# Kernel tuning notes

Hardware: AMD Instinct MI355X
Metric: run time of the kernel (lower is better)

## Reference

```python
import jax, jax.numpy as jnp
import numpy as np

D_MODEL = 512
H = 8
DK = D_MODEL // H  # 64


def setup_inputs() -> dict:
    key = jax.random.key(0)
    ks = jax.random.split(key, 8)
    B, S = 2, 4096
    q = jax.random.normal(ks[0], (B, S, D_MODEL), dtype=jnp.float32)
    k = jax.random.normal(ks[1], (B, S, D_MODEL), dtype=jnp.float32)
    v = jax.random.normal(ks[2], (B, S, D_MODEL), dtype=jnp.float32)
    # per-head projection weights, torch nn.Linear layout [out, in], stacked over heads
    scale = 1.0 / np.sqrt(D_MODEL)
    Wq = jax.random.uniform(ks[3], (H, DK, D_MODEL), jnp.float32, -scale, scale)
    Wk = jax.random.uniform(ks[4], (H, DK, D_MODEL), jnp.float32, -scale, scale)
    Wv = jax.random.uniform(ks[5], (H, DK, D_MODEL), jnp.float32, -scale, scale)
    Wo = jax.random.uniform(ks[6], (D_MODEL, D_MODEL), jnp.float32, -scale, scale)
    # causal mask (True = keep), matches masked_fill(mask.logical_not(), -inf)
    mask = jnp.tril(jnp.ones((S, S), dtype=jnp.bool_))
    return {"q": q, "k": k, "v": v, "Wq": Wq, "Wk": Wk, "Wv": Wv, "Wo": Wo, "mask": mask}


def reference(q, k, v, Wq, Wk, Wv, Wo, mask):
    # per-head projections (stacked): x @ W^T for each head -> [B, H, S, DK]
    qh = jnp.einsum('bsd,hed->bhse', q, Wq)
    kh = jnp.einsum('bsd,hed->bhse', k, Wk)
    vh = jnp.einsum('bsd,hed->bhse', v, Wv)
    scaling = 1.0 / np.sqrt(DK)
    scores = jnp.einsum('bhse,bhte->bhst', qh, kh) * scaling  # [B,H,S,S]
    scores = jnp.where(mask, scores, -jnp.inf)
    attn = jax.nn.softmax(scores, axis=-1)
    heads = jnp.einsum('bhst,bhte->bhse', attn, vh)  # [B,H,S,DK]
    B, _, S, _ = heads.shape
    concat = jnp.transpose(heads, (0, 2, 1, 3)).reshape(B, S, D_MODEL)
    return concat @ Wo.T
```

## Files before the change

### kernel.cpp

```cpp
#include <hip/hip_runtime.h>
#include <hip/hip_bf16.h>
#include <math.h>

typedef __bf16 bf16_t;
typedef __bf16 bf16x8 __attribute__((ext_vector_type(8)));
typedef __bf16 bf16x4 __attribute__((ext_vector_type(4)));
typedef short short4v __attribute__((ext_vector_type(4)));
typedef float f32x4 __attribute__((ext_vector_type(4)));

__device__ __forceinline__ f32x4 mfma_k32(bf16x8 a, bf16x8 b, f32x4 c) {
    return __builtin_amdgcn_mfma_f32_16x16x32_bf16(a, b, c, 0, 0, 0);
}

__device__ __forceinline__ f32x4 mfma_k16(bf16x4 a, bf16x4 b, f32x4 c) {
#if __has_builtin(__builtin_amdgcn_mfma_f32_16x16x16_bf16)
    return __builtin_amdgcn_mfma_f32_16x16x16_bf16(a, b, c, 0, 0, 0);
#elif __has_builtin(__builtin_amdgcn_mfma_f32_16x16x16bf16_1k)
    short4v as, bs;
    __builtin_memcpy(&as, &a, 8);
    __builtin_memcpy(&bs, &b, 8);
    return __builtin_amdgcn_mfma_f32_16x16x16bf16_1k(as, bs, c, 0, 0, 0);
#else
    f32x4 d = c;
    asm volatile("v_mfma_f32_16x16x16_bf16 %0, %1, %2, %0" : "+v"(d) : "v"(a), "v"(b));
    return d;
#endif
}

__device__ __forceinline__ void async16(const bf16_t* g, __bf16* l) {
    __builtin_amdgcn_global_load_lds(
        (const __attribute__((address_space(1))) void*)g,
        (__attribute__((address_space(3))) void*)l, 16, 0, 0);
}

__device__ __forceinline__ int swz_col(int col, int row) {
    return (col & ~63) | ((((col >> 3) & 7) ^ (row & 7)) << 3) | (col & 7);
}

__global__ __launch_bounds__(256) void cvt_x(const float* __restrict__ q,
                                             const float* __restrict__ k,
                                             const float* __restrict__ v,
                                             bf16_t* __restrict__ qc,
                                             bf16_t* __restrict__ kc,
                                             bf16_t* __restrict__ vc) {
    size_t i = ((size_t)blockIdx.x * 256 + threadIdx.x) * 8;
    int row = (int)(i >> 9), col = (int)(i & 511);
    size_t di = (size_t)row * 512 + swz_col(col, row);
    float4 a0 = *(const float4*)(q + i), a1 = *(const float4*)(q + i + 4);
    float4 b0 = *(const float4*)(k + i), b1 = *(const float4*)(k + i + 4);
    float4 c0 = *(const float4*)(v + i), c1 = *(const float4*)(v + i + 4);
    bf16x8 qo, ko, vo;
    qo[0]=(__bf16)a0.x; qo[1]=(__bf16)a0.y; qo[2]=(__bf16)a0.z; qo[3]=(__bf16)a0.w;
    qo[4]=(__bf16)a1.x; qo[5]=(__bf16)a1.y; qo[6]=(__bf16)a1.z; qo[7]=(__bf16)a1.w;
    ko[0]=(__bf16)b0.x; ko[1]=(__bf16)b0.y; ko[2]=(__bf16)b0.z; ko[3]=(__bf16)b0.w;
    ko[4]=(__bf16)b1.x; ko[5]=(__bf16)b1.y; ko[6]=(__bf16)b1.z; ko[7]=(__bf16)b1.w;
    vo[0]=(__bf16)c0.x; vo[1]=(__bf16)c0.y; vo[2]=(__bf16)c0.z; vo[3]=(__bf16)c0.w;
    vo[4]=(__bf16)c1.x; vo[5]=(__bf16)c1.y; vo[6]=(__bf16)c1.z; vo[7]=(__bf16)c1.w;
    *(bf16x8*)(qc + di) = qo;
    *(bf16x8*)(kc + di) = ko;
    *(bf16x8*)(vc + di) = vo;
}

__global__ __launch_bounds__(256) void cvt_w(const float* __restrict__ Wq,
                                             const float* __restrict__ Wk,
                                             const float* __restrict__ Wv,
                                             const float* __restrict__ Wo,
                                             bf16_t* __restrict__ Wc) {
    const int m = blockIdx.y;
    const float* src = m == 0 ? Wq : m == 1 ? Wk : m == 2 ? Wv : Wo;
    const float sc = (m == 0) ? 0.125f * 1.44269504088896f : 1.0f;
    size_t i = ((size_t)blockIdx.x * 256 + threadIdx.x) * 8;
    int row = (int)(i >> 9), col = (int)(i & 511);
    float4 a0 = *(const float4*)(src + i), a1 = *(const float4*)(src + i + 4);
    bf16x8 o;
    o[0]=(__bf16)(a0.x*sc); o[1]=(__bf16)(a0.y*sc); o[2]=(__bf16)(a0.z*sc); o[3]=(__bf16)(a0.w*sc);
    o[4]=(__bf16)(a1.x*sc); o[5]=(__bf16)(a1.y*sc); o[6]=(__bf16)(a1.z*sc); o[7]=(__bf16)(a1.w*sc);
    *(bf16x8*)(Wc + (size_t)m * 262144 + (size_t)row * 512 + swz_col(col, row)) = o;
}

template<int MODE>
__global__ __launch_bounds__(256) void gemm_nt(const bf16_t* __restrict__ A,
                                               const bf16_t* __restrict__ B,
                                               void* __restrict__ outp) {
    __shared__ __bf16 Asm[64 * 64];
    __shared__ __bf16 Bsm[64 * 64];
    const int tid  = threadIdx.x;
    const int wave = tid >> 6;
    const int lane = tid & 63;
    const int quad = lane >> 4;
    const int l16  = lane & 15;
    const int swz  = l16 & 7;
    const int m0 = blockIdx.x * 64;
    const int n0 = blockIdx.y * 64;
    const int r8 = lane >> 3;
    const int c8 = (lane & 7) * 8;

    f32x4 acc[4];
    for (int i = 0; i < 4; ++i) acc[i] = (f32x4){0.f, 0.f, 0.f, 0.f};

    for (int kt = 0; kt < 512; kt += 64) {
        __syncthreads();
        for (int j = 0; j < 2; ++j) {
            int row = wave * 16 + j * 8 + r8;
            async16(A + (size_t)(m0 + row) * 512 + kt + c8, &Asm[(wave * 16 + j * 8) * 64]);
            async16(B + (size_t)(n0 + row) * 512 + kt + c8, &Bsm[(wave * 16 + j * 8) * 64]);
        }
        __syncthreads();

        for (int ks = 0; ks < 2; ++ks) {
            bf16x8 afr = *(const bf16x8*)&Asm[(wave * 16 + l16) * 64 + ((ks * 4 + quad) ^ swz) * 8];
            for (int nt = 0; nt < 4; ++nt) {
                bf16x8 bfr = *(const bf16x8*)&Bsm[(nt * 16 + l16) * 64 + ((ks * 4 + quad) ^ swz) * 8];
                acc[nt] = mfma_k32(afr, bfr, acc[nt]);
            }
        }
    }

    if (MODE == 0) {
        bf16_t* out = (bf16_t*)outp;
        for (int nt = 0; nt < 4; ++nt) {
            int e = n0 + nt * 16 + l16;
            int h = e >> 6, el = e & 63;
            for (int r = 0; r < 4; ++r) {
                int row = m0 + wave * 16 + quad * 4 + r;
                int b = row >> 12, s = row & 4095;
                int elp = (((el >> 3) ^ (row & 7)) << 3) | (el & 7);
                out[(((size_t)(b * 8 + h)) * 4096 + s) * 64 + elp] = (bf16_t)acc[nt][r];
            }
        }
    } else if (MODE == 1) {
        bf16_t* out = (bf16_t*)outp;
        for (int nt = 0; nt < 4; ++nt) {
            int s_g = n0 + nt * 16 + l16;
            int b = s_g >> 12, sl = s_g & 4095;
            int f = 16 * (l16 >> 2) + 4 * nt + (l16 & 3);
            for (int r = 0; r < 4; ++r) {
                int e_g = m0 + wave * 16 + quad * 4 + r;
                int h = e_g >> 6, el = e_g & 63;
                int p = (sl & ~63) | ((((f >> 3) ^ (e_g & 7)) & 7) << 3) | (f & 7);
                out[(((size_t)(b * 8 + h)) * 64 + el) * 4096 + p] = (bf16_t)acc[nt][r];
            }
        }
    } else {
        float* out = (float*)outp;
        for (int nt = 0; nt < 4; ++nt) {
            int n = n0 + nt * 16 + l16;
            for (int r = 0; r < 4; ++r) {
                int row = m0 + wave * 16 + quad * 4 + r;
                out[(size_t)row * 512 + n] = acc[nt][r];
            }
        }
    }
}

__global__ __launch_bounds__(256) void attn_kernel(const bf16_t* __restrict__ qh,
                                                   const bf16_t* __restrict__ kh,
                                                   const bf16_t* __restrict__ vh,
                                                   bf16_t* __restrict__ ao) {
    __shared__ __bf16 Ksm[64 * 64];
    __shared__ __bf16 VTsm[64 * 64];
    const int tid  = threadIdx.x;
    const int wave = tid >> 6;
    const int lane = tid & 63;
    const int quad = lane >> 4;
    const int l16  = lane & 15;
    const int swz  = l16 & 7;
    const int bh   = blockIdx.y;
    const size_t base = (size_t)bh * 4096 * 64;
    const int r8 = lane >> 3;
    const int c8 = (lane & 7) * 8;
    const int b = bh >> 3, h = bh & 7;

    for (int leg = 0; leg < 2; ++leg) {
        const int qt = leg ? (63 - (int)blockIdx.x) : (int)blockIdx.x;
        const int q0 = qt * 64;
        const int qrow = wave * 16 + l16;
        const bf16_t* qp = qh + base + (size_t)(q0 + qrow) * 64;
        bf16x8 qf0 = *(const bf16x8*)(qp + ((quad ^ swz) * 8));
        bf16x8 qf1 = *(const bf16x8*)(qp + (((4 + quad) ^ swz) * 8));

        f32x4 o[4];
        for (int i = 0; i < 4; ++i) o[i] = (f32x4){0.f, 0.f, 0.f, 0.f};
        float lsum = 0.f;

        for (int jt = 0; jt <= qt; ++jt) {
            const int j0 = jt * 64;
            __syncthreads();
            for (int j = 0; j < 2; ++j) {
                int row = wave * 16 + j * 8 + r8;
                async16(kh + base + (size_t)(j0 + row) * 64 + c8,
                        &Ksm[(wave * 16 + j * 8) * 64]);
                async16(vh + (size_t)(bh * 64 + row) * 4096 + j0 + c8,
                        &VTsm[(wave * 16 + j * 8) * 64]);
            }
            __syncthreads();

            f32x4 st[4];
            for (int nt = 0; nt < 4; ++nt) {
                bf16x8 kf0 = *(const bf16x8*)&Ksm[(nt * 16 + l16) * 64 + ((quad ^ swz) * 8)];
                bf16x8 kf1 = *(const bf16x8*)&Ksm[(nt * 16 + l16) * 64 + (((4 + quad) ^ swz) * 8)];
                f32x4 z = (f32x4){0.f, 0.f, 0.f, 0.f};
                z = mfma_k32(kf0, qf0, z);
                z = mfma_k32(kf1, qf1, z);
                st[nt] = z;
            }

            bf16x4 pf[4];
            if (jt == qt) {
                for (int nt = 0; nt < 4; ++nt)
                    for (int r = 0; r < 4; ++r) {
                        int key = nt * 16 + quad * 4 + r;
                        float p = (key <= qrow) ? exp2f(st[nt][r]) : 0.f;
                        lsum += p;
                        pf[nt][r] = (bf16_t)p;
                    }
            } else {
                for (int nt = 0; nt < 4; ++nt)
                    for (int r = 0; r < 4; ++r) {
                        float p = exp2f(st[nt][r]);
                        lsum += p;
                        pf[nt][r] = (bf16_t)p;
                    }
            }

            for (int dt = 0; dt < 4; ++dt) {
                for (int kt2 = 0; kt2 < 2; ++kt2) {
                    bf16x8 vf = *(const bf16x8*)&VTsm[(dt * 16 + l16) * 64 + (((2 * quad + kt2) ^ swz) * 8)];
                    bf16x4 vlo = {vf[0], vf[1], vf[2], vf[3]};
                    bf16x4 vhi = {vf[4], vf[5], vf[6], vf[7]};
                    o[dt] = mfma_k16(pf[2 * kt2], vlo, o[dt]);
                    o[dt] = mfma_k16(pf[2 * kt2 + 1], vhi, o[dt]);
                }
            }
        }

        lsum += __shfl_xor(lsum, 16);
        lsum += __shfl_xor(lsum, 32);
        float linv[4];
        for (int r = 0; r < 4; ++r) linv[r] = 1.0f / __shfl(lsum, quad * 4 + r);
        for (int r = 0; r < 4; ++r) {
            int s_g = q0 + wave * 16 + quad * 4 + r;
            size_t rowoff = ((size_t)(b * 4096 + s_g)) * 512;
            for (int dt = 0; dt < 4; ++dt) {
                int el = dt * 16 + l16;
                int elp = (((el >> 3) ^ (s_g & 7)) << 3) | (el & 7);
                ao[rowoff + h * 64 + elp] = (bf16_t)(o[dt][r] * linv[r]);
            }
        }
    }
}

extern "C" void kernel_launch(void* const* d_in, const int* in_sizes, int n_in,
                              void* d_out, int out_size, void* d_ws, size_t ws_size,
                              hipStream_t stream) {
    const float* q  = (const float*)d_in[0];
    const float* k  = (const float*)d_in[1];
    const float* v  = (const float*)d_in[2];
    const float* Wq = (const float*)d_in[3];
    const float* Wk = (const float*)d_in[4];
    const float* Wv = (const float*)d_in[5];
    const float* Wo = (const float*)d_in[6];
    float* out = (float*)d_out;

    bf16_t* ws = (bf16_t*)d_ws;
    const size_t R = (size_t)8192 * 512;
    bf16_t* qc = ws;
    bf16_t* kc = ws + R;
    bf16_t* vc = ws + 2 * R;
    bf16_t* qh = ws + 3 * R;
    bf16_t* Wc = ws + 4 * R;
    bf16_t* kh = qc;
    bf16_t* vh = kc;
    bf16_t* ao = vc;

    dim3 bb(256);
    cvt_x<<<dim3(2048), bb, 0, stream>>>(q, k, v, qc, kc, vc);
    cvt_w<<<dim3(128, 4), bb, 0, stream>>>(Wq, Wk, Wv, Wo, Wc);
    gemm_nt<0><<<dim3(128, 8), bb, 0, stream>>>(qc, Wc, qh);
    gemm_nt<0><<<dim3(128, 8), bb, 0, stream>>>(kc, Wc + 262144, kh);
    gemm_nt<1><<<dim3(8, 128), bb, 0, stream>>>(Wc + 2 * 262144, vc, vh);
    attn_kernel<<<dim3(32, 16), bb, 0, stream>>>(qh, kh, vh, ao);
    gemm_nt<2><<<dim3(128, 8), bb, 0, stream>>>(ao, Wc + 3 * 262144, out);
}
```

Baseline: 271.9 us.

## Fuse Q/K/V projections into one launch, widen GEMM tiles, unpair attention legs

Merges the three projection GEMMs into one kernel indexed by blockIdx.z and widens the N tile from 64 to 128 with eight accumulators per wave, for both the projection and output GEMMs. The V projection is now computed as x·Wv^T and written transposed with packed 4-wide stores instead of a separately oriented GEMM. Attention no longer pairs a short and a long query tile per block; it launches 64 blocks per head instead, which may hurt load balance. It also moves qh/kh into the output buffer as scratch, cutting launches and reusing A tiles more, at the cost of more registers per thread.

```diff
diff --git a/kernel.cpp b/kernel.cpp
--- a/kernel.cpp
+++ b/kernel.cpp
@@ -78,12 +78,16 @@
     *(bf16x8*)(Wc + (size_t)m * 262144 + (size_t)row * 512 + swz_col(col, row)) = o;
 }
 
-template<int MODE>
-__global__ __launch_bounds__(256) void gemm_nt(const bf16_t* __restrict__ A,
-                                               const bf16_t* __restrict__ B,
-                                               void* __restrict__ outp) {
+__global__ __launch_bounds__(256) void proj_fused(const bf16_t* __restrict__ xs,
+                                                  const bf16_t* __restrict__ Wc,
+                                                  bf16_t* __restrict__ qh,
+                                                  bf16_t* __restrict__ kh,
+                                                  bf16_t* __restrict__ vh) {
     __shared__ __bf16 Asm[64 * 64];
-    __shared__ __bf16 Bsm[64 * 64];
+    __shared__ __bf16 Bsm[128 * 64];
+    const int z    = blockIdx.z;
+    const bf16_t* A = xs + (size_t)z * 4194304;
+    const bf16_t* B = Wc + (size_t)z * 262144;
     const int tid  = threadIdx.x;
     const int wave = tid >> 6;
     const int lane = tid & 63;
@@ -91,34 +95,35 @@
     const int l16  = lane & 15;
     const int swz  = l16 & 7;
     const int m0 = blockIdx.x * 64;
-    const int n0 = blockIdx.y * 64;
+    const int n0 = blockIdx.y * 128;
     const int r8 = lane >> 3;
     const int c8 = (lane & 7) * 8;
 
-    f32x4 acc[4];
-    for (int i = 0; i < 4; ++i) acc[i] = (f32x4){0.f, 0.f, 0.f, 0.f};
+    f32x4 acc[8];
+    for (int i = 0; i < 8; ++i) acc[i] = (f32x4){0.f, 0.f, 0.f, 0.f};
 
     for (int kt = 0; kt < 512; kt += 64) {
         __syncthreads();
-        for (int j = 0; j < 2; ++j) {
-            int row = wave * 16 + j * 8 + r8;
-            async16(A + (size_t)(m0 + row) * 512 + kt + c8, &Asm[(wave * 16 + j * 8) * 64]);
-            async16(B + (size_t)(n0 + row) * 512 + kt + c8, &Bsm[(wave * 16 + j * 8) * 64]);
-        }
+        for (int j = 0; j < 2; ++j)
+            async16(A + (size_t)(m0 + wave * 16 + j * 8 + r8) * 512 + kt + c8,
+                    &Asm[(wave * 16 + j * 8) * 64]);
+        for (int j = 0; j < 4; ++j)
+            async16(B + (size_t)(n0 + wave * 32 + j * 8 + r8) * 512 + kt + c8,
+                    &Bsm[(wave * 32 + j * 8) * 64]);
         __syncthreads();
 
         for (int ks = 0; ks < 2; ++ks) {
             bf16x8 afr = *(const bf16x8*)&Asm[(wave * 16 + l16) * 64 + ((ks * 4 + quad) ^ swz) * 8];
-            for (int nt = 0; nt < 4; ++nt) {
+            for (int nt = 0; nt < 8; ++nt) {
                 bf16x8 bfr = *(const bf16x8*)&Bsm[(nt * 16 + l16) * 64 + ((ks * 4 + quad) ^ swz) * 8];
                 acc[nt] = mfma_k32(afr, bfr, acc[nt]);
             }
         }
     }
 
-    if (MODE == 0) {
-        bf16_t* out = (bf16_t*)outp;
-        for (int nt = 0; nt < 4; ++nt) {
+    if (z < 2) {
+        bf16_t* out = z ? kh : qh;
+        for (int nt = 0; nt < 8; ++nt) {
             int e = n0 + nt * 16 + l16;
             int h = e >> 6, el = e & 63;
             for (int r = 0; r < 4; ++r) {
@@ -128,27 +133,66 @@
                 out[(((size_t)(b * 8 + h)) * 4096 + s) * 64 + elp] = (bf16_t)acc[nt][r];
             }
         }
-    } else if (MODE == 1) {
-        bf16_t* out = (bf16_t*)outp;
-        for (int nt = 0; nt < 4; ++nt) {
-            int s_g = n0 + nt * 16 + l16;
-            int b = s_g >> 12, sl = s_g & 4095;
-            int f = 16 * (l16 >> 2) + 4 * nt + (l16 & 3);
-            for (int r = 0; r < 4; ++r) {
-                int e_g = m0 + wave * 16 + quad * 4 + r;
-                int h = e_g >> 6, el = e_g & 63;
-                int p = (sl & ~63) | ((((f >> 3) ^ (e_g & 7)) & 7) << 3) | (f & 7);
-                out[(((size_t)(b * 8 + h)) * 64 + el) * 4096 + p] = (bf16_t)acc[nt][r];
+    } else {
+        const int bb = m0 >> 12;
+        const int sbase = m0 & 4095 & ~63;
+        const int chunk = 2 * quad + (wave >> 1);
+        const int elo   = 4 * (wave & 1);
+        for (int nt = 0; nt < 8; ++nt) {
+            int e_g = n0 + nt * 16 + l16;
+            int h = e_g >> 6, el = e_g & 63;
+            int col = sbase + ((chunk ^ (e_g & 7)) << 3) + elo;
+            bf16x4 pk;
+            pk[0] = (bf16_t)acc[nt][0]; pk[1] = (bf16_t)acc[nt][1];
+            pk[2] = (bf16_t)acc[nt][2]; pk[3] = (bf16_t)acc[nt][3];
+            *(bf16x4*)&vh[(((size_t)(bb * 8 + h)) * 64 + el) * 4096 + col] = pk;
+        }
+    }
+}
+
+__global__ __launch_bounds__(256) void gemm_final(const bf16_t* __restrict__ A,
+                                                  const bf16_t* __restrict__ B,
+                                                  float* __restrict__ out) {
+    __shared__ __bf16 Asm[64 * 64];
+    __shared__ __bf16 Bsm[128 * 64];
+    const int tid  = threadIdx.x;
+    const int wave = tid >> 6;
+    const int lane = tid & 63;
+    const int quad = lane >> 4;
+    const int l16  = lane & 15;
+    const int swz  = l16 & 7;
+    const int m0 = blockIdx.x * 64;
+    const int n0 = blockIdx.y * 128;
+    const int r8 = lane >> 3;
+    const int c8 = (lane & 7) * 8;
+
+    f32x4 acc[8];
+    for (int i = 0; i < 8; ++i) acc[i] = (f32x4){0.f, 0.f, 0.f, 0.f};
+
+    for (int kt = 0; kt < 512; kt += 64) {
+        __syncthreads();
+        for (int j = 0; j < 2; ++j)
+            async16(A + (size_t)(m0 + wave * 16 + j * 8 + r8) * 512 + kt + c8,
+                    &Asm[(wave * 16 + j * 8) * 64]);
+        for (int j = 0; j < 4; ++j)
+            async16(B + (size_t)(n0 + wave * 32 + j * 8 + r8) * 512 + kt + c8,
+                    &Bsm[(wave * 32 + j * 8) * 64]);
+        __syncthreads();
+
+        for (int ks = 0; ks < 2; ++ks) {
+            bf16x8 afr = *(const bf16x8*)&Asm[(wave * 16 + l16) * 64 + ((ks * 4 + quad) ^ swz) * 8];
+            for (int nt = 0; nt < 8; ++nt) {
+                bf16x8 bfr = *(const bf16x8*)&Bsm[(nt * 16 + l16) * 64 + ((ks * 4 + quad) ^ swz) * 8];
+                acc[nt] = mfma_k32(afr, bfr, acc[nt]);
             }
         }
-    } else {
-        float* out = (float*)outp;
-        for (int nt = 0; nt < 4; ++nt) {
-            int n = n0 + nt * 16 + l16;
-            for (int r = 0; r < 4; ++r) {
-                int row = m0 + wave * 16 + quad * 4 + r;
-                out[(size_t)row * 512 + n] = acc[nt][r];
-            }
+    }
+
+    for (int nt = 0; nt < 8; ++nt) {
+        int n = n0 + nt * 16 + l16;
+        for (int r = 0; r < 4; ++r) {
+            int row = m0 + wave * 16 + quad * 4 + r;
+            out[(size_t)row * 512 + n] = acc[nt][r];
         }
     }
 }
@@ -171,81 +215,79 @@
     const int c8 = (lane & 7) * 8;
     const int b = bh >> 3, h = bh & 7;
 
-    for (int leg = 0; leg < 2; ++leg) {
-        const int qt = leg ? (63 - (int)blockIdx.x) : (int)blockIdx.x;
-        const int q0 = qt * 64;
-        const int qrow = wave * 16 + l16;
-        const bf16_t* qp = qh + base + (size_t)(q0 + qrow) * 64;
-        bf16x8 qf0 = *(const bf16x8*)(qp + ((quad ^ swz) * 8));
-        bf16x8 qf1 = *(const bf16x8*)(qp + (((4 + quad) ^ swz) * 8));
-
-        f32x4 o[4];
-        for (int i = 0; i < 4; ++i) o[i] = (f32x4){0.f, 0.f, 0.f, 0.f};
-        float lsum = 0.f;
-
-        for (int jt = 0; jt <= qt; ++jt) {
-            const int j0 = jt * 64;
-            __syncthreads();
-            for (int j = 0; j < 2; ++j) {
-                int row = wave * 16 + j * 8 + r8;
-                async16(kh + base + (size_t)(j0 + row) * 64 + c8,
-                        &Ksm[(wave * 16 + j * 8) * 64]);
-                async16(vh + (size_t)(bh * 64 + row) * 4096 + j0 + c8,
-                        &VTsm[(wave * 16 + j * 8) * 64]);
+    const int qt = 63 - (int)blockIdx.x;
+    const int q0 = qt * 64;
+    const int qrow = wave * 16 + l16;
+    const bf16_t* qp = qh + base + (size_t)(q0 + qrow) * 64;
+    bf16x8 qf0 = *(const bf16x8*)(qp + ((quad ^ swz) * 8));
+    bf16x8 qf1 = *(const bf16x8*)(qp + (((4 + quad) ^ swz) * 8));
+
+    f32x4 o[4];
+    for (int i = 0; i < 4; ++i) o[i] = (f32x4){0.f, 0.f, 0.f, 0.f};
+    float lsum = 0.f;
+
+    for (int jt = 0; jt <= qt; ++jt) {
+        const int j0 = jt * 64;
+        __syncthreads();
+        for (int j = 0; j < 2; ++j) {
+            int row = wave * 16 + j * 8 + r8;
+            async16(kh + base + (size_t)(j0 + row) * 64 + c8,
+                    &Ksm[(wave * 16 + j * 8) * 64]);
+            async16(vh + (size_t)(bh * 64 + row) * 4096 + j0 + c8,
+                    &VTsm[(wave * 16 + j * 8) * 64]);
+        }
+        __syncthreads();
+
+        f32x4 st[4];
+        for (int nt = 0; nt < 4; ++nt) {
+            bf16x8 kf0 = *(const bf16x8*)&Ksm[(nt * 16 + l16) * 64 + ((quad ^ swz) * 8)];
+            bf16x8 kf1 = *(const bf16x8*)&Ksm[(nt * 16 + l16) * 64 + (((4 + quad) ^ swz) * 8)];
+            f32x4 z = (f32x4){0.f, 0.f, 0.f, 0.f};
+            z = mfma_k32(kf0, qf0, z);
+            z = mfma_k32(kf1, qf1, z);
+            st[nt] = z;
+        }
+
+        bf16x4 pf[4];
+        if (jt == qt) {
+            for (int nt = 0; nt < 4; ++nt)
+                for (int r = 0; r < 4; ++r) {
+                    int key = nt * 16 + quad * 4 + r;
+                    float p = (key <= qrow) ? exp2f(st[nt][r]) : 0.f;
+                    lsum += p;
+                    pf[nt][r] = (bf16_t)p;
+                }
+        } else {
+            for (int nt = 0; nt < 4; ++nt)
+                for (int r = 0; r < 4; ++r) {
+                    float p = exp2f(st[nt][r]);
+                    lsum += p;
+                    pf[nt][r] = (bf16_t)p;
+                }
+        }
+
+        for (int dt = 0; dt < 4; ++dt) {
+            for (int kt2 = 0; kt2 < 2; ++kt2) {
+                bf16x8 vf = *(const bf16x8*)&VTsm[(dt * 16 + l16) * 64 + (((2 * quad + kt2) ^ swz) * 8)];
+                bf16x4 vlo = {vf[0], vf[1], vf[2], vf[3]};
+                bf16x4 vhi = {vf[4], vf[5], vf[6], vf[7]};
+                o[dt] = mfma_k16(pf[2 * kt2], vlo, o[dt]);
+                o[dt] = mfma_k16(pf[2 * kt2 + 1], vhi, o[dt]);
             }
-            __syncthreads();
-
-            f32x4 st[4];
-            for (int nt = 0; nt < 4; ++nt) {
-                bf16x8 kf0 = *(const bf16x8*)&Ksm[(nt * 16 + l16) * 64 + ((quad ^ swz) * 8)];
-                bf16x8 kf1 = *(const bf16x8*)&Ksm[(nt * 16 + l16) * 64 + (((4 + quad) ^ swz) * 8)];
-                f32x4 z = (f32x4){0.f, 0.f, 0.f, 0.f};
-                z = mfma_k32(kf0, qf0, z);
-                z = mfma_k32(kf1, qf1, z);
-                st[nt] = z;
-            }
-
-            bf16x4 pf[4];
-            if (jt == qt) {
-                for (int nt = 0; nt < 4; ++nt)
-                    for (int r = 0; r < 4; ++r) {
-                        int key = nt * 16 + quad * 4 + r;
-                        float p = (key <= qrow) ? exp2f(st[nt][r]) : 0.f;
-                        lsum += p;
-                        pf[nt][r] = (bf16_t)p;
-                    }
-            } else {
-                for (int nt = 0; nt < 4; ++nt)
-                    for (int r = 0; r < 4; ++r) {
-                        float p = exp2f(st[nt][r]);
-                        lsum += p;
-                        pf[nt][r] = (bf16_t)p;
-                    }
-            }
-
-            for (int dt = 0; dt < 4; ++dt) {
-                for (int kt2 = 0; kt2 < 2; ++kt2) {
-                    bf16x8 vf = *(const bf16x8*)&VTsm[(dt * 16 + l16) * 64 + (((2 * quad + kt2) ^ swz) * 8)];
-                    bf16x4 vlo = {vf[0], vf[1], vf[2], vf[3]};
-                    bf16x4 vhi = {vf[4], vf[5], vf[6], vf[7]};
-                    o[dt] = mfma_k16(pf[2 * kt2], vlo, o[dt]);
-                    o[dt] = mfma_k16(pf[2 * kt2 + 1], vhi, o[dt]);
-                }
-            }
-        }
-
-        lsum += __shfl_xor(lsum, 16);
-        lsum += __shfl_xor(lsum, 32);
-        float linv[4];
-        for (int r = 0; r < 4; ++r) linv[r] = 1.0f / __shfl(lsum, quad * 4 + r);
-        for (int r = 0; r < 4; ++r) {
-            int s_g = q0 + wave * 16 + quad * 4 + r;
-            size_t rowoff = ((size_t)(b * 4096 + s_g)) * 512;
-            for (int dt = 0; dt < 4; ++dt) {
-                int el = dt * 16 + l16;
-                int elp = (((el >> 3) ^ (s_g & 7)) << 3) | (el & 7);
-                ao[rowoff + h * 64 + elp] = (bf16_t)(o[dt][r] * linv[r]);
-            }
+        }
+    }
+
+    lsum += __shfl_xor(lsum, 16);
+    lsum += __shfl_xor(lsum, 32);
+    float linv[4];
+    for (int r = 0; r < 4; ++r) linv[r] = 1.0f / __shfl(lsum, quad * 4 + r);
+    for (int r = 0; r < 4; ++r) {
+        int s_g = q0 + wave * 16 + quad * 4 + r;
+        size_t rowoff = ((size_t)(b * 4096 + s_g)) * 512;
+        for (int dt = 0; dt < 4; ++dt) {
+            int el = dt * 16 + l16;
+            int elp = (((el >> 3) ^ (s_g & 7)) << 3) | (el & 7);
+            ao[rowoff + h * 64 + elp] = (bf16_t)(o[dt][r] * linv[r]);
         }
     }
 }
@@ -267,18 +309,16 @@
     bf16_t* qc = ws;
     bf16_t* kc = ws + R;
     bf16_t* vc = ws + 2 * R;
-    bf16_t* qh = ws + 3 * R;
+    bf16_t* vh = ws + 3 * R;
     bf16_t* Wc = ws + 4 * R;
-    bf16_t* kh = qc;
-    bf16_t* vh = kc;
-    bf16_t* ao = vc;
+    bf16_t* qh = (bf16_t*)d_out;
+    bf16_t* kh = (bf16_t*)d_out + R;
+    bf16_t* ao = qc;
 
     dim3 bb(256);
     cvt_x<<<dim3(2048), bb, 0, stream>>>(q, k, v, qc, kc, vc);
     cvt_w<<<dim3(128, 4), bb, 0, stream>>>(Wq, Wk, Wv, Wo, Wc);
-    gemm_nt<0><<<dim3(128, 8), bb, 0, stream>>>(qc, Wc, qh);
-    gemm_nt<0><<<dim3(128, 8), bb, 0, stream>>>(kc, Wc + 262144, kh);
-    gemm_nt<1><<<dim3(8, 128), bb, 0, stream>>>(Wc + 2 * 262144, vc, vh);
-    attn_kernel<<<dim3(32, 16), bb, 0, stream>>>(qh, kh, vh, ao);
-    gemm_nt<2><<<dim3(128, 8), bb, 0, stream>>>(ao, Wc + 3 * 262144, out);
-}
+    proj_fused<<<dim3(128, 4, 3), bb, 0, stream>>>(ws, Wc, qh, kh, vh);
+    attn_kernel<<<dim3(64, 16), bb, 0, stream>>>(qh, kh, vh, ao);
+    gemm_final<<<dim3(128, 4), bb, 0, stream>>>(ao, Wc + 3 * 262144, out);
+}
```

Measured after the change: 299.9 us. 10.3% more time.
